# Kernel tuning notes

Hardware: AMD Instinct MI355X
Metric: run time of the kernel (lower is better)

## Reference

```python
import jax, jax.numpy as jnp
import numpy as np

N, TI, TO1 = 8, 200, 51
V, E, H, J, L = 1024, 512, 512, 512, 3
ENC_D = 512


def setup_inputs() -> dict:
    key = jax.random.key(0)
    ks = jax.random.split(key, 11)
    s = lambda k, shape, sc: jax.random.normal(k, shape, jnp.float32) * sc
    return {
        "enc_out": s(ks[0], (N, TI, ENC_D), 1.0),
        "tgt_pad": jax.random.randint(ks[1], (N, TO1), 0, V),
        "embed": s(ks[2], (V, E), 0.02),          # nn.Embedding weight
        "w_ih": s(ks[3], (L, 4 * H, E), 0.04),    # LSTM input-hidden (gate order i,f,g,o)
        "w_hh": s(ks[4], (L, 4 * H, H), 0.04),    # LSTM hidden-hidden
        "b_ih": s(ks[5], (L, 4 * H), 0.04),
        "b_hh": s(ks[6], (L, 4 * H), 0.04),
        "enc_w": s(ks[7], (J, ENC_D), 0.04),      # enc_proj (no bias)
        "dec_w": s(ks[8], (J, H), 0.04),          # dec_proj weight
        "dec_b": s(ks[9], (J,), 0.04),            # dec_proj bias
        "out_w": s(ks[10], (V, J), 0.04),         # output (no bias)
    }


def lstm_layer(x, wih, whh, bih, bhh):
    # x: [N, T, E] -> [N, T, H]; PyTorch LSTM gate order i, f, g, o
    n = x.shape[0]
    h0 = jnp.zeros((n, whh.shape[1]), x.dtype)
    c0 = jnp.zeros_like(h0)
    gin = jnp.einsum('nte,ge->ntg', x, wih) + bih + bhh  # precompute input contributions

    def step(carry, g_t):
        h, c = carry
        g = g_t + h @ whh.T
        i, f, gg, o = jnp.split(g, 4, axis=-1)
        c = jax.nn.sigmoid(f) * c + jax.nn.sigmoid(i) * jnp.tanh(gg)
        h = jax.nn.sigmoid(o) * jnp.tanh(c)
        return (h, c), h

    _, hs = jax.lax.scan(step, (h0, c0), jnp.swapaxes(gin, 0, 1))
    return jnp.swapaxes(hs, 0, 1)


def reference(enc_out, tgt_pad, embed, w_ih, w_hh, b_ih, b_hh, enc_w, dec_w, dec_b, out_w):
    # embedding lookup
    x = embed[tgt_pad]                                   # [N, To+1, E]
    # 3-layer unidirectional LSTM
    for l in range(w_ih.shape[0]):
        x = lstm_layer(x, w_ih[l], w_hh[l], b_ih[l], b_hh[l])
    # projections
    enc_p = jnp.einsum('ntd,jd->ntj', enc_out, enc_w)    # [N, Ti, J]
    dec_p = jnp.einsum('nud,jd->nuj', x, dec_w) + dec_b  # [N, To+1, J]
    # joint: broadcast add -> tanh -> output linear (no bias)
    add = enc_p[:, :, None, :] + dec_p[:, None, :, :]    # [N, Ti, To+1, J]
    return jnp.einsum('ntuj,vj->ntuv', jnp.tanh(add), out_w)  # [N, Ti, To+1, V]
```

## Files before the change

kernel.cpp:

```cpp
#include <hip/hip_runtime.h>
#include <cstdint>
#include <cstddef>

typedef __attribute__((ext_vector_type(4))) float f32x4;
typedef __attribute__((ext_vector_type(8))) short bf16x8;
typedef __attribute__((ext_vector_type(8))) unsigned short u16x8;
typedef __attribute__((ext_vector_type(4))) float float4v;
typedef __attribute__((ext_vector_type(2))) unsigned long long u64x2;
typedef unsigned long long ull;

#define NB   8
#define TIN  200
#define TO1  51
#define VSZ  1024
#define HSZ  512
static constexpr int MJOINT = NB * TIN * TO1;
static constexpr int MROWS  = TO1 * NB;

static constexpr size_t B_ENCBF = 0;
static constexpr size_t B_ENCW  = B_ENCBF + 1664ull*512*2;
static constexpr size_t B_DECW  = B_ENCW  + 512ull*512*2;
static constexpr size_t B_OUTW  = B_DECW  + 512ull*512*2;
static constexpr size_t B_WIH   = B_OUTW  + 1024ull*512*2;
static constexpr size_t B_WHH   = B_WIH   + 3ull*2048*512*2;
static constexpr size_t B_XTR   = B_WHH   + 3ull*2048*512*2;
static constexpr size_t B_BSUM  = B_XTR   + 4ull*408*512*2;
static constexpr size_t B_FLAGS = B_BSUM  + 3ull*2048*4;
static constexpr size_t B_ENCP  = B_FLAGS + 8192;
static constexpr size_t B_DECP  = B_ENCP  + 1664ull*512*4;
static constexpr size_t B_ABUF  = B_DECP  + 512ull*512*4;

__device__ __forceinline__ unsigned short f2bf(float f) {
  union { float f; unsigned u; } v; v.f = f;
  unsigned r = v.u + 0x7FFFu + ((v.u >> 16) & 1u);
  return (unsigned short)(r >> 16);
}
__device__ __forceinline__ float fast_tanh(float x) {
  float t = __expf(2.0f * x);
  return 1.0f - 2.0f / (t + 1.0f);
}
__device__ __forceinline__ float fast_sig(float x) {
  return 1.0f / (1.0f + __expf(-x));
}
__device__ __forceinline__ void gll16(const void* g, void* l) {
  __builtin_amdgcn_global_load_lds(
      (const __attribute__((address_space(1))) unsigned int*)g,
      (__attribute__((address_space(3))) unsigned int*)l, 16, 0, 0);
}
__device__ __forceinline__ void cvt8(const float* s, unsigned short* d) {
  const float4v* sp = (const float4v*)s;
  float4v x = sp[0], y = sp[1];
  u16x8 o;
  o[0]=f2bf(x[0]); o[1]=f2bf(x[1]); o[2]=f2bf(x[2]); o[3]=f2bf(x[3]);
  o[4]=f2bf(y[0]); o[5]=f2bf(y[1]); o[6]=f2bf(y[2]); o[7]=f2bf(y[3]);
  *(u16x8*)d = o;
}
#define ALOAD(P)     __hip_atomic_load((P), __ATOMIC_RELAXED, __HIP_MEMORY_SCOPE_AGENT)
#define ASTORE(P, V) __hip_atomic_store((P), (V), __ATOMIC_RELAXED, __HIP_MEMORY_SCOPE_AGENT)

static constexpr int N_ENC  = 102400;
static constexpr int N_ENCW = 32768;
static constexpr int N_DECW = 32768;
static constexpr int N_OUTW = 65536;
static constexpr int N_WIH  = 393216;
static constexpr int P0 = N_ENC, P1 = P0+N_ENCW, P2 = P1+N_DECW, P3 = P2+N_OUTW,
                     P4 = P3+N_WIH;

__global__ __launch_bounds__(256) void prep_all(const float* __restrict__ enc,
                                                const float* __restrict__ encw,
                                                const float* __restrict__ decw,
                                                const float* __restrict__ outw,
                                                const float* __restrict__ wih,
                                                const float* __restrict__ whh,
                                                const float* __restrict__ emb,
                                                const int* __restrict__ tgt,
                                                const float* __restrict__ bih,
                                                const float* __restrict__ bhh,
                                                unsigned short* __restrict__ d_enc,
                                                unsigned short* __restrict__ d_encw,
                                                unsigned short* __restrict__ d_decw,
                                                unsigned short* __restrict__ d_outw,
                                                unsigned short* __restrict__ d_wih,
                                                unsigned short* __restrict__ d_whh,
                                                unsigned short* __restrict__ x0,
                                                float* __restrict__ bsum,
                                                int* __restrict__ flags) {
  if (blockIdx.x == 0 && threadIdx.x < 97) flags[threadIdx.x * 16] = 0;
  if (blockIdx.x >= 4086) {
    int i = (blockIdx.x - 4086) * 2048 + threadIdx.x * 8;
#pragma unroll
    for (int k = 0; k < 8; ++k) bsum[i + k] = bih[i + k] + bhh[i + k];
    return;
  }
  if (blockIdx.x >= 3984) {
    int idx = (blockIdx.x - 3984) * 256 + threadIdx.x;
    if (idx >= MROWS * 64) return;
    int m = idx >> 6, kc = (idx & 63) * 8;
    int t = m >> 3, n = m & 7;
    int v = tgt[n * TO1 + t];
    cvt8(emb + (size_t)v * 512 + kc, x0 + (size_t)m * 512 + kc);
    return;
  }
  int i = blockIdx.x * 256 + threadIdx.x;
  const float* s; unsigned short* d; int rel;
  if      (i < P0) { s = enc;  d = d_enc;  rel = i; }
  else if (i < P1) { s = encw; d = d_encw; rel = i - P0; }
  else if (i < P2) { s = decw; d = d_decw; rel = i - P1; }
  else if (i < P3) { s = outw; d = d_outw; rel = i - P2; }
  else if (i < P4) { s = wih;  d = d_wih;  rel = i - P3; }
  else             { s = whh;  d = d_whh;  rel = i - P4; }
  cvt8(s + (size_t)rel * 8, d + (size_t)rel * 8);
}

__global__ __launch_bounds__(512) void gemm256(const unsigned short* __restrict__ A,
                                               const unsigned short* __restrict__ B,
                                               float* __restrict__ C,
                                               int M, int N, int K) {
  __shared__ __align__(16) unsigned short lds[2][2][16384];
  const int tid = threadIdx.x;
  const int wave = tid >> 6, lane = tid & 63;
  const int lr = lane & 15, lg = lane >> 4;
  const int wr = (wave >> 2) * 128;
  const int wc = (wave & 3) * 64;

  const int nwg = gridDim.x * gridDim.y;
  const int id = blockIdx.y * gridDim.x + blockIdx.x;
  const int q = nwg >> 3, r = nwg & 7, xcd = id & 7, rest = id >> 3;
  const int nid = (xcd < r ? xcd * (q + 1) : r * (q + 1) + (xcd - r) * q) + rest;
  const size_t n0 = (size_t)(nid % gridDim.x) * 256;
  const size_t m0 = (size_t)(nid / gridDim.x) * 256;

  f32x4 acc[8][4];
#pragma unroll
  for (int i = 0; i < 8; ++i)
#pragma unroll
    for (int j = 0; j < 4; ++j) acc[i][j] = (f32x4){0.f, 0.f, 0.f, 0.f};

#define STGH(bf, kt, h)                                                                 \
  do {                                                                                  \
    const unsigned short* SRC_ = ((h) < 2) ? A : B;                                     \
    const size_t base_ = ((h) < 2) ? m0 : n0;                                           \
    _Pragma("unroll") for (int u = 0; u < 2; ++u) {                                     \
      const int idx2 = u * 512 + tid;                                                   \
      const int rloc = (idx2 >> 3) + (((h) & 1) << 7);                                  \
      const int ch = (idx2 & 7) ^ (rloc & 7);                                           \
      gll16(SRC_ + (base_ + rloc) * (size_t)K + (kt) + ch * 8,                          \
            &lds[bf][(h) >> 1][((((h) & 1) << 10) + u * 512 + wave * 64) * 8]);         \
    }                                                                                   \
  } while (0)

  STGH(0, 0, 0); STGH(0, 0, 1); STGH(0, 0, 2); STGH(0, 0, 3);

  int cur = 0;
  for (int t = 0; t < 8; ++t) {
    const int nxt = cur ^ 1;
    const unsigned short* As_ = lds[cur][0];
    const unsigned short* Bs_ = lds[cur][1];
    bf16x8 b[4][2];
#pragma unroll
    for (int p = 0; p < 4; ++p) {
      if (t + 1 < 8) STGH(nxt, (t + 1) * 64, p);
      if (p == 0) {
        if (t + 1 < 8) asm volatile("s_waitcnt vmcnt(2)" ::: "memory");
        else           asm volatile("s_waitcnt vmcnt(0)" ::: "memory");
        __builtin_amdgcn_s_barrier();
#pragma unroll
        for (int j = 0; j < 4; ++j) {
          const int rb = wc + j * 16 + lr;
          const int sw = rb & 7;
          b[j][0] = *(const bf16x8*)&Bs_[rb * 64 + ((lg ^ sw) << 3)];
          b[j][1] = *(const bf16x8*)&Bs_[rb * 64 + (((4 + lg) ^ sw) << 3)];
        }
      }
      bf16x8 a[2][2];
#pragma unroll
      for (int i2 = 0; i2 < 2; ++i2) {
        const int ra = wr + (p * 2 + i2) * 16 + lr;
        const int swa = ra & 7;
        a[i2][0] = *(const bf16x8*)&As_[ra * 64 + ((lg ^ swa) << 3)];
        a[i2][1] = *(const bf16x8*)&As_[ra * 64 + (((4 + lg) ^ swa) << 3)];
      }
      __builtin_amdgcn_s_setprio(1);
#pragma unroll
      for (int i2 = 0; i2 < 2; ++i2) {
        const int i = p * 2 + i2;
#pragma unroll
        for (int j = 0; j < 4; ++j) {
          acc[i][j] = __builtin_amdgcn_mfma_f32_16x16x32_bf16(a[i2][0], b[j][0], acc[i][j], 0, 0, 0);
          acc[i][j] = __builtin_amdgcn_mfma_f32_16x16x32_bf16(a[i2][1], b[j][1], acc[i][j], 0, 0, 0);
        }
      }
      __builtin_amdgcn_s_setprio(0);
      __builtin_amdgcn_s_barrier();
    }
    cur = nxt;
  }
#undef STGH

#pragma unroll
  for (int i = 0; i < 8; ++i) {
#pragma unroll
    for (int q2 = 0; q2 < 4; ++q2) {
      const long m = (long)m0 + wr + i * 16 + lg * 4 + q2;
      if (m < M) {
        float* crow = C + (size_t)m * N + n0 + wc;
#pragma unroll
        for (int j = 0; j < 4; ++j) crow[j * 16 + lr] = acc[i][j][q2];
      }
    }
  }
}

__global__ __launch_bounds__(256) void mega_kernel(const unsigned short* __restrict__ wih,
                                                   const unsigned short* __restrict__ whh,
                                                   const float* __restrict__ bsum,
                                                   unsigned short* __restrict__ xtr,
                                                   int* __restrict__ flags,
                                                   const unsigned short* __restrict__ eA,
                                                   const unsigned short* __restrict__ eB,
                                                   float* __restrict__ eC,
                                                   const unsigned short* __restrict__ decw,
                                                   const float* __restrict__ dec_b,
                                                   const float* __restrict__ encp,
                                                   unsigned short* __restrict__ abuf) {
  __shared__ __align__(16) unsigned short w_s[64 * 1024];
  __shared__ __align__(16) unsigned short x_s[8 * 512];
  __shared__ __align__(16) unsigned short h_s[8 * 512];
  __shared__ float gates_s[4][8][16];

  const int tid = threadIdx.x;
  const int wave = tid >> 6, lane = tid & 63;
  const int lr = lane & 15, lg = lane >> 4;
  const int r7 = lr & 7;

  if (blockIdx.x >= 148) {
    const int wkr = blockIdx.x - 148;
    unsigned short* h3_s = x_s;
    float* decp_row = (float*)w_s;
    const unsigned short* xtr3 = xtr + 3ull * MROWS * 512;
#pragma unroll 1
    for (int k = 0; k < 4; ++k) {
      const int j = wkr + 102 * k;
      const int u = j >> 3;
      const int p = j & 7;
      if (wave == 0) {
        for (;;) {
          bool ok = true;
          if (lane < 32) ok = ALOAD(&flags[(64 + lane) * 16]) >= u + 1;
          else if (lane == 32) ok = ALOAD(&flags[96 * 16]) >= 52;
          if (__all(ok)) break;
          __builtin_amdgcn_s_sleep(1);
        }
      }
      __syncthreads();
      {
        const int sr2 = tid >> 5, sc2 = tid & 31;
        const ull* ph = (const ull*)(xtr3 + ((size_t)u * 8 + sr2) * 512);
#pragma unroll
        for (int k2 = 0; k2 < 2; ++k2) {
          const int c_ = sc2 + k2 * 32;
          ull v0 = ALOAD(ph + c_ * 2), v1 = ALOAD(ph + c_ * 2 + 1);
          *(u64x2*)&h3_s[sr2 * 512 + ((c_ ^ sr2) << 3)] = (u64x2){v0, v1};
        }
      }
      __syncthreads();
      {
        const int colbase = wave * 128;
#pragma unroll
        for (int ct = 0; ct < 8; ++ct) {
          f32x4 acc = (f32x4){0.f, 0.f, 0.f, 0.f};
          const int col = colbase + ct * 16 + lr;
#pragma unroll
          for (int c16 = 0; c16 < 16; ++c16) {
            const int cc = c16 * 4 + lg;
            bf16x8 av = *(const bf16x8*)&h3_s[r7 * 512 + ((cc ^ r7) << 3)];
            bf16x8 bv = *(const bf16x8*)&decw[(size_t)col * 512 + cc * 8];
            acc = __builtin_amdgcn_mfma_f32_16x16x32_bf16(av, bv, acc, 0, 0, 0);
          }
#pragma unroll
          for (int q2 = 0; q2 < 4; ++q2)
            if (lg * 4 + q2 == p) decp_row[col] = acc[q2] + dec_b[col];
        }
      }
      __syncthreads();
      {
        const int tr = tid >> 6;
        const int colc = (lane) * 8;
        for (int pass = 0; pass < 50; ++pass) {
          const int nt = p * 200 + pass * 4 + tr;
          const float4v* pe = (const float4v*)(encp + (size_t)nt * 512 + colc);
          float4v e0 = pe[0], e1 = pe[1];
          u16x8 o;
#pragma unroll
          for (int w2 = 0; w2 < 4; ++w2) {
            o[w2]     = f2bf(fast_tanh(e0[w2] + decp_row[colc + w2]));
            o[4 + w2] = f2bf(fast_tanh(e1[w2] + decp_row[colc + 4 + w2]));
          }
          *(u16x8*)&abuf[((size_t)nt * TO1 + u) * 512 + colc] = o;
        }
      }
      __syncthreads();
    }
    return;
  }

  if (blockIdx.x >= 96) {
    unsigned short* eld = w_s;
    const int g = blockIdx.x - 96;
    const int wm = (wave >> 1) * 64, wn = (wave & 1) * 64;
    const int xsl = (lg ^ (lr & 3)) << 3;
    const int nwg = 52;
    const int q = nwg >> 3, r = nwg & 7, xcd = g & 7, rest = g >> 3;
    const int nid = (xcd < r ? xcd * (q + 1) : r * (q + 1) + (xcd - r) * q) + rest;
    const size_t n0 = (size_t)(nid & 3) * 128;
    const size_t m0 = (size_t)(nid >> 2) * 128;

    f32x4 acc[4][4];
#pragma unroll
    for (int i = 0; i < 4; ++i)
#pragma unroll
      for (int j = 0; j < 4; ++j) acc[i][j] = (f32x4){0.f, 0.f, 0.f, 0.f};

#define ESTG(bf, kt)                                                                   \
    do {                                                                               \
      _Pragma("unroll") for (int u = 0; u < 2; ++u) {                                  \
        const int s = u * 256 + tid;                                                   \
        const int row_ = s >> 2;                                                       \
        const int ch = (s & 3) ^ (row_ & 3);                                           \
        gll16(eA + (m0 + row_) * 512 + (kt) + ch * 8,                                  \
              &eld[(bf) * 8192 + (u * 256 + wave * 64) * 8]);                          \
      }                                                                                \
      _Pragma("unroll") for (int u = 0; u < 2; ++u) {                                  \
        const int s = u * 256 + tid;                                                   \
        const int row_ = s >> 2;                                                       \
        const int ch = (s & 3) ^ (row_ & 3);                                           \
        gll16(eB + (n0 + row_) * 512 + (kt) + ch * 8,                                  \
              &eld[(bf) * 8192 + 4096 + (u * 256 + wave * 64) * 8]);                   \
      }                                                                                \
    } while (0)

    int cur = 0;
    ESTG(0, 0);
    for (int t = 0; t < 16; ++t) {
      if (t + 1 < 16) {
        ESTG(cur ^ 1, (t + 1) * 32);
        asm volatile("s_waitcnt vmcnt(4)" ::: "memory");
      } else {
        asm volatile("s_waitcnt vmcnt(0)" ::: "memory");
      }
      __builtin_amdgcn_s_barrier();
      const unsigned short* As_ = eld + cur * 8192;
      const unsigned short* Bs_ = As_ + 4096;
      bf16x8 a[4], b[4];
#pragma unroll
      for (int i = 0; i < 4; ++i) a[i] = *(const bf16x8*)&As_[(wm + i * 16 + lr) * 32 + xsl];
#pragma unroll
      for (int j = 0; j < 4; ++j) b[j] = *(const bf16x8*)&Bs_[(wn + j * 16 + lr) * 32 + xsl];
      __builtin_amdgcn_s_setprio(1);
#pragma unroll
      for (int i = 0; i < 4; ++i)
#pragma unroll
        for (int j = 0; j < 4; ++j)
          acc[i][j] = __builtin_amdgcn_mfma_f32_16x16x32_bf16(a[i], b[j], acc[i][j], 0, 0, 0);
      __builtin_amdgcn_s_setprio(0);
      __builtin_amdgcn_s_barrier();
      cur ^= 1;
    }
#undef ESTG

    const int rq = lg * 4;
#pragma unroll
    for (int j = 0; j < 4; ++j) {
      const int col = (int)n0 + wn + j * 16 + lr;
#pragma unroll
      for (int i = 0; i < 4; ++i) {
#pragma unroll
        for (int q2 = 0; q2 < 4; ++q2) {
          const long m = (long)m0 + wm + i * 16 + rq + q2;
          ASTORE(&eC[(size_t)m * 512 + col], acc[i][j][q2]);
        }
      }
    }
    asm volatile("s_waitcnt vmcnt(0)" ::: "memory");
    __syncthreads();
    if (tid == 0)
      __hip_atomic_fetch_add(&flags[96 * 16], 1, __ATOMIC_RELAXED, __HIP_MEMORY_SCOPE_AGENT);
    return;
  }

  const int l = blockIdx.x >> 5;
  const int b32 = blockIdx.x & 31;
  const int hid0 = b32 << 4;
  const int rw = wave * 16 + lr;

  {
    const int rl = tid >> 2;
    const int qt = tid & 3;
    const size_t R = (size_t)l * 2048 + (size_t)(rl >> 4) * 512 + hid0 + (rl & 15);
    const unsigned short* s0 = wih + R * 512;
    const unsigned short* s1 = whh + R * 512;
#pragma unroll
    for (int i = 0; i < 32; ++i) {
      int c = qt * 32 + i;
      bf16x8 wv = (c < 64) ? *(const bf16x8*)&s0[c * 8] : *(const bf16x8*)&s1[(c - 64) * 8];
      *(bf16x8*)&w_s[rl * 1024 + ((c ^ (rl & 7)) << 3)] = wv;
    }
  }
  const float bias = bsum[(size_t)l * 2048 + (size_t)wave * 512 + hid0 + lr];

  const unsigned short* xin = xtr + (size_t)l * MROWS * 512;
  unsigned short* xout = xtr + (size_t)(l + 1) * MROWS * 512;
  float c_reg = 0.f;
  const int srow = tid >> 5;
  const int sc = tid & 31;
  __syncthreads();

  f32x4 ax0, ax1;

  if (l > 0) {
    if (wave == 0) {
      for (;;) {
        bool ok_ = true;
        if (lane < 32)
          ok_ = ALOAD(&flags[((l - 1) * 32 + lane) * 16]) >= 1;
        if (__all(ok_)) break;
        __builtin_amdgcn_s_sleep(1);
      }
    }
  }
  __syncthreads();
  {
    const ull* px = (const ull*)(xin + (size_t)srow * 512);
#pragma unroll
    for (int k_ = 0; k_ < 2; ++k_) {
      const int c_ = sc + k_ * 32;
      ull v0 = ALOAD(px + c_ * 2), v1 = ALOAD(px + c_ * 2 + 1);
      *(u64x2*)&x_s[srow * 512 + ((c_ ^ srow) << 3)] = (u64x2){v0, v1};
    }
  }
  __syncthreads();
  ax0 = (f32x4){0.f, 0.f, 0.f, 0.f};
  ax1 = (f32x4){0.f, 0.f, 0.f, 0.f};
#pragma unroll
  for (int c16 = 0; c16 < 16; ++c16) {
    const int cc = c16 * 4 + lg;
    bf16x8 av = *(const bf16x8*)&x_s[r7 * 512 + ((cc ^ r7) << 3)];
    bf16x8 bv = *(const bf16x8*)&w_s[rw * 1024 + ((cc ^ r7) << 3)];
    if (c16 & 1) ax1 = __builtin_amdgcn_mfma_f32_16x16x32_bf16(av, bv, ax1, 0, 0, 0);
    else         ax0 = __builtin_amdgcn_mfma_f32_16x16x32_bf16(av, bv, ax0, 0, 0, 0);
  }

  for (int t = 0; t < TO1; ++t) {
    const bool doH = (t > 0);
    const bool doX = (t + 1 < TO1);
    if (doH || (doX && l > 0)) {
      if (wave == 0) {
        for (;;) {
          bool ok_ = true;
          if (lane < 32) {
            if (doH) ok_ = ALOAD(&flags[(l * 32 + lane) * 16]) >= t;
          } else {
            if (doX && l > 0)
              ok_ = ALOAD(&flags[((l - 1) * 32 + (lane - 32)) * 16]) >= t + 2;
          }
          if (__all(ok_)) break;
          __builtin_amdgcn_s_sleep(1);
        }
      }
    }
    __syncthreads();

    {
      ull vh[4], vx[4];
      const ull* ph = (const ull*)(xout + ((size_t)(t - 1) * 8 + srow) * 512);
      const ull* px = (const ull*)(xin + ((size_t)(t + 1) * 8 + srow) * 512);
#pragma unroll
      for (int k_ = 0; k_ < 2; ++k_) {
        const int c_ = sc + k_ * 32;
        if (doH) { vh[2 * k_] = ALOAD(ph + c_ * 2); vh[2 * k_ + 1] = ALOAD(ph + c_ * 2 + 1); }
        if (doX) { vx[2 * k_] = ALOAD(px + c_ * 2); vx[2 * k_ + 1] = ALOAD(px + c_ * 2 + 1); }
      }
#pragma unroll
      for (int k_ = 0; k_ < 2; ++k_) {
        const int c_ = sc + k_ * 32;
        if (doH) *(u64x2*)&h_s[srow * 512 + ((c_ ^ srow) << 3)] = (u64x2){vh[2 * k_], vh[2 * k_ + 1]};
        if (doX) *(u64x2*)&x_s[srow * 512 + ((c_ ^ srow) << 3)] = (u64x2){vx[2 * k_], vx[2 * k_ + 1]};
      }
    }
    __syncthreads();

    f32x4 acc0 = ax0, acc1 = ax1;
    if (doH) {
#pragma unroll
      for (int c16 = 0; c16 < 16; ++c16) {
        const int cc = c16 * 4 + lg;
        bf16x8 av = *(const bf16x8*)&h_s[r7 * 512 + ((cc ^ r7) << 3)];
        bf16x8 bv = *(const bf16x8*)&w_s[rw * 1024 + (((64 + cc) ^ r7) << 3)];
        if (c16 & 1) acc1 = __builtin_amdgcn_mfma_f32_16x16x32_bf16(av, bv, acc1, 0, 0, 0);
        else         acc0 = __builtin_amdgcn_mfma_f32_16x16x32_bf16(av, bv, acc0, 0, 0, 0);
      }
    }

    {
      f32x4 g = acc0 + acc1;
      const int nb4 = lg * 4;
#pragma unroll
      for (int q2 = 0; q2 < 4; ++q2) {
        int n = nb4 + q2;
        if (n < 8) gates_s[wave][n][lr] = g[q2] + bias;
      }
    }
    __syncthreads();
    if (tid < 128) {
      const int n = tid >> 4, j = tid & 15;
      float gi = gates_s[0][n][j], gf = gates_s[1][n][j];
      float gg = gates_s[2][n][j], go = gates_s[3][n][j];
      c_reg = fast_sig(gf) * c_reg + fast_sig(gi) * fast_tanh(gg);
      float ht = fast_sig(go) * fast_tanh(c_reg);
      float htn = __shfl_down(ht, 1);
      if (!(j & 1)) {
        unsigned pk = (unsigned)f2bf(ht) | ((unsigned)f2bf(htn) << 16);
        ASTORE((unsigned*)(xout + ((size_t)t * 8 + n) * 512 + hid0 + j), pk);
      }
    }
    asm volatile("s_waitcnt vmcnt(0)" ::: "memory");
    __syncthreads();
    if (tid == 0)
      ASTORE(&flags[(l * 32 + b32) * 16], t + 1);

    if (doX) {
      ax0 = (f32x4){0.f, 0.f, 0.f, 0.f};
      ax1 = (f32x4){0.f, 0.f, 0.f, 0.f};
#pragma unroll
      for (int c16 = 0; c16 < 16; ++c16) {
        const int cc = c16 * 4 + lg;
        bf16x8 av = *(const bf16x8*)&x_s[r7 * 512 + ((cc ^ r7) << 3)];
        bf16x8 bv = *(const bf16x8*)&w_s[rw * 1024 + ((cc ^ r7) << 3)];
        if (c16 & 1) ax1 = __builtin_amdgcn_mfma_f32_16x16x32_bf16(av, bv, ax1, 0, 0, 0);
        else         ax0 = __builtin_amdgcn_mfma_f32_16x16x32_bf16(av, bv, ax0, 0, 0, 0);
      }
    }
  }
}

extern "C" void kernel_launch(void* const* d_in, const int* in_sizes, int n_in,
                              void* d_out, int out_size, void* d_ws, size_t ws_size,
                              hipStream_t stream) {
  (void)in_sizes; (void)n_in; (void)out_size; (void)ws_size;
  const float* enc_out = (const float*)d_in[0];
  const int*   tgt     = (const int*)d_in[1];
  const float* embed   = (const float*)d_in[2];
  const float* w_ih    = (const float*)d_in[3];
  const float* w_hh    = (const float*)d_in[4];
  const float* b_ih    = (const float*)d_in[5];
  const float* b_hh    = (const float*)d_in[6];
  const float* enc_w   = (const float*)d_in[7];
  const float* dec_w   = (const float*)d_in[8];
  const float* dec_b   = (const float*)d_in[9];
  const float* out_w   = (const float*)d_in[10];

  char* ws = (char*)d_ws;
  unsigned short* enc_bf  = (unsigned short*)(ws + B_ENCBF);
  unsigned short* encw_bf = (unsigned short*)(ws + B_ENCW);
  unsigned short* decw_bf = (unsigned short*)(ws + B_DECW);
  unsigned short* outw_bf = (unsigned short*)(ws + B_OUTW);
  unsigned short* wih_bf  = (unsigned short*)(ws + B_WIH);
  unsigned short* whh_bf  = (unsigned short*)(ws + B_WHH);
  unsigned short* xtr     = (unsigned short*)(ws + B_XTR);
  float* bsum  = (float*)(ws + B_BSUM);
  int*   flags = (int*)(ws + B_FLAGS);
  float* encp  = (float*)(ws + B_ENCP);
  unsigned short* abuf = (unsigned short*)(ws + B_ABUF);
  float* Cout  = (float*)d_out;

  prep_all<<<4089, 256, 0, stream>>>(enc_out, enc_w, dec_w, out_w, w_ih, w_hh,
                                     embed, tgt, b_ih, b_hh,
                                     enc_bf, encw_bf, decw_bf, outw_bf, wih_bf, whh_bf,
                                     xtr, bsum, flags);

  mega_kernel<<<250, 256, 0, stream>>>(wih_bf, whh_bf, bsum, xtr, flags,
                                       enc_bf, encw_bf, encp,
                                       decw_bf, dec_b, encp, abuf);

  gemm256<<<dim3(4, 319), 512, 0, stream>>>(abuf, outw_bf, Cout, MJOINT, VSZ, 512);
}
```

Before: 325.7 us.

## Fuse output GEMM into persistent mega kernel with work-stealing tiles overlapping the LSTM

Removes the separate output GEMM launch and folds it into the persistent mega kernel. Blocks grab tiles through an atomic counter once they finish their LSTM, projection or joint roles. Each tile waits on per-timestep readiness flags, so the joint GEMM can start while later LSTM steps still run. The abuf layout becomes u-major so tiles map to contiguous timesteps, and blocks grow to 512 threads with only the first 256 doing the old work. This risks lower occupancy, spin-wait contention, and interference with the latency-critical recurrence.

```diff
diff --git a/kernel.cpp b/kernel.cpp
--- a/kernel.cpp
+++ b/kernel.cpp
@@ -16,6 +16,7 @@
 #define HSZ  512
 static constexpr int MJOINT = NB * TIN * TO1;
 static constexpr int MROWS  = TO1 * NB;
+static constexpr int NTK    = 319 * 4;
 
 static constexpr size_t B_ENCBF = 0;
 static constexpr size_t B_ENCW  = B_ENCBF + 1664ull*512*2;
@@ -57,6 +58,7 @@
 }
 #define ALOAD(P)     __hip_atomic_load((P), __ATOMIC_RELAXED, __HIP_MEMORY_SCOPE_AGENT)
 #define ASTORE(P, V) __hip_atomic_store((P), (V), __ATOMIC_RELAXED, __HIP_MEMORY_SCOPE_AGENT)
+#define AADD(P, V)   __hip_atomic_fetch_add((P), (V), __ATOMIC_RELAXED, __HIP_MEMORY_SCOPE_AGENT)
 
 static constexpr int N_ENC  = 102400;
 static constexpr int N_ENCW = 32768;
@@ -85,7 +87,10 @@
                                                 unsigned short* __restrict__ x0,
                                                 float* __restrict__ bsum,
                                                 int* __restrict__ flags) {
-  if (blockIdx.x == 0 && threadIdx.x < 97) flags[threadIdx.x * 16] = 0;
+  if (blockIdx.x == 0) {
+#pragma unroll
+    for (int k = 0; k < 8; ++k) flags[threadIdx.x * 8 + k] = 0;
+  }
   if (blockIdx.x >= 4086) {
     int i = (blockIdx.x - 4086) * 2048 + threadIdx.x * 8;
 #pragma unroll
@@ -112,106 +117,7 @@
   cvt8(s + (size_t)rel * 8, d + (size_t)rel * 8);
 }
 
-__global__ __launch_bounds__(512) void gemm256(const unsigned short* __restrict__ A,
-                                               const unsigned short* __restrict__ B,
-                                               float* __restrict__ C,
-                                               int M, int N, int K) {
-  __shared__ __align__(16) unsigned short lds[2][2][16384];
-  const int tid = threadIdx.x;
-  const int wave = tid >> 6, lane = tid & 63;
-  const int lr = lane & 15, lg = lane >> 4;
-  const int wr = (wave >> 2) * 128;
-  const int wc = (wave & 3) * 64;
-
-  const int nwg = gridDim.x * gridDim.y;
-  const int id = blockIdx.y * gridDim.x + blockIdx.x;
-  const int q = nwg >> 3, r = nwg & 7, xcd = id & 7, rest = id >> 3;
-  const int nid = (xcd < r ? xcd * (q + 1) : r * (q + 1) + (xcd - r) * q) + rest;
-  const size_t n0 = (size_t)(nid % gridDim.x) * 256;
-  const size_t m0 = (size_t)(nid / gridDim.x) * 256;
-
-  f32x4 acc[8][4];
-#pragma unroll
-  for (int i = 0; i < 8; ++i)
-#pragma unroll
-    for (int j = 0; j < 4; ++j) acc[i][j] = (f32x4){0.f, 0.f, 0.f, 0.f};
-
-#define STGH(bf, kt, h)                                                                 \
-  do {                                                                                  \
-    const unsigned short* SRC_ = ((h) < 2) ? A : B;                                     \
-    const size_t base_ = ((h) < 2) ? m0 : n0;                                           \
-    _Pragma("unroll") for (int u = 0; u < 2; ++u) {                                     \
-      const int idx2 = u * 512 + tid;                                                   \
-      const int rloc = (idx2 >> 3) + (((h) & 1) << 7);                                  \
-      const int ch = (idx2 & 7) ^ (rloc & 7);                                           \
-      gll16(SRC_ + (base_ + rloc) * (size_t)K + (kt) + ch * 8,                          \
-            &lds[bf][(h) >> 1][((((h) & 1) << 10) + u * 512 + wave * 64) * 8]);         \
-    }                                                                                   \
-  } while (0)
-
-  STGH(0, 0, 0); STGH(0, 0, 1); STGH(0, 0, 2); STGH(0, 0, 3);
-
-  int cur = 0;
-  for (int t = 0; t < 8; ++t) {
-    const int nxt = cur ^ 1;
-    const unsigned short* As_ = lds[cur][0];
-    const unsigned short* Bs_ = lds[cur][1];
-    bf16x8 b[4][2];
-#pragma unroll
-    for (int p = 0; p < 4; ++p) {
-      if (t + 1 < 8) STGH(nxt, (t + 1) * 64, p);
-      if (p == 0) {
-        if (t + 1 < 8) asm volatile("s_waitcnt vmcnt(2)" ::: "memory");
-        else           asm volatile("s_waitcnt vmcnt(0)" ::: "memory");
-        __builtin_amdgcn_s_barrier();
-#pragma unroll
-        for (int j = 0; j < 4; ++j) {
-          const int rb = wc + j * 16 + lr;
-          const int sw = rb & 7;
-          b[j][0] = *(const bf16x8*)&Bs_[rb * 64 + ((lg ^ sw) << 3)];
-          b[j][1] = *(const bf16x8*)&Bs_[rb * 64 + (((4 + lg) ^ sw) << 3)];
-        }
-      }
-      bf16x8 a[2][2];
-#pragma unroll
-      for (int i2 = 0; i2 < 2; ++i2) {
-        const int ra = wr + (p * 2 + i2) * 16 + lr;
-        const int swa = ra & 7;
-        a[i2][0] = *(const bf16x8*)&As_[ra * 64 + ((lg ^ swa) << 3)];
-        a[i2][1] = *(const bf16x8*)&As_[ra * 64 + (((4 + lg) ^ swa) << 3)];
-      }
-      __builtin_amdgcn_s_setprio(1);
-#pragma unroll
-      for (int i2 = 0; i2 < 2; ++i2) {
-        const int i = p * 2 + i2;
-#pragma unroll
-        for (int j = 0; j < 4; ++j) {
-          acc[i][j] = __builtin_amdgcn_mfma_f32_16x16x32_bf16(a[i2][0], b[j][0], acc[i][j], 0, 0, 0);
-          acc[i][j] = __builtin_amdgcn_mfma_f32_16x16x32_bf16(a[i2][1], b[j][1], acc[i][j], 0, 0, 0);
-        }
-      }
-      __builtin_amdgcn_s_setprio(0);
-      __builtin_amdgcn_s_barrier();
-    }
-    cur = nxt;
-  }
-#undef STGH
-
-#pragma unroll
-  for (int i = 0; i < 8; ++i) {
-#pragma unroll
-    for (int q2 = 0; q2 < 4; ++q2) {
-      const long m = (long)m0 + wr + i * 16 + lg * 4 + q2;
-      if (m < M) {
-        float* crow = C + (size_t)m * N + n0 + wc;
-#pragma unroll
-        for (int j = 0; j < 4; ++j) crow[j * 16 + lr] = acc[i][j][q2];
-      }
-    }
-  }
-}
-
-__global__ __launch_bounds__(256) void mega_kernel(const unsigned short* __restrict__ wih,
+__global__ __launch_bounds__(512) void mega_kernel(const unsigned short* __restrict__ wih,
                                                    const unsigned short* __restrict__ whh,
                                                    const float* __restrict__ bsum,
                                                    unsigned short* __restrict__ xtr,
@@ -222,11 +128,14 @@
                                                    const unsigned short* __restrict__ decw,
                                                    const float* __restrict__ dec_b,
                                                    const float* __restrict__ encp,
-                                                   unsigned short* __restrict__ abuf) {
+                                                   unsigned short* __restrict__ abuf,
+                                                   const unsigned short* __restrict__ outw,
+                                                   float* __restrict__ Cout) {
   __shared__ __align__(16) unsigned short w_s[64 * 1024];
   __shared__ __align__(16) unsigned short x_s[8 * 512];
   __shared__ __align__(16) unsigned short h_s[8 * 512];
   __shared__ float gates_s[4][8][16];
+  __shared__ int tk_s;
 
   const int tid = threadIdx.x;
   const int wave = tid >> 6, lane = tid & 63;
@@ -247,13 +156,13 @@
         for (;;) {
           bool ok = true;
           if (lane < 32) ok = ALOAD(&flags[(64 + lane) * 16]) >= u + 1;
-          else if (lane == 32) ok = ALOAD(&flags[96 * 16]) >= 52;
+          else if (lane == 32) ok = ALOAD(&flags[1536]) >= 52;
           if (__all(ok)) break;
           __builtin_amdgcn_s_sleep(1);
         }
       }
       __syncthreads();
-      {
+      if (tid < 256) {
         const int sr2 = tid >> 5, sc2 = tid & 31;
         const ull* ph = (const ull*)(xtr3 + ((size_t)u * 8 + sr2) * 512);
 #pragma unroll
@@ -264,7 +173,7 @@
         }
       }
       __syncthreads();
-      {
+      if (wave < 4) {
         const int colbase = wave * 128;
 #pragma unroll
         for (int ct = 0; ct < 8; ++ct) {
@@ -285,9 +194,9 @@
       __syncthreads();
       {
         const int tr = tid >> 6;
-        const int colc = (lane) * 8;
-        for (int pass = 0; pass < 50; ++pass) {
-          const int nt = p * 200 + pass * 4 + tr;
+        const int colc = lane * 8;
+        for (int pass = 0; pass < 25; ++pass) {
+          const int nt = p * 200 + pass * 8 + tr;
           const float4v* pe = (const float4v*)(encp + (size_t)nt * 512 + colc);
           float4v e0 = pe[0], e1 = pe[1];
           u16x8 o;
@@ -296,15 +205,17 @@
             o[w2]     = f2bf(fast_tanh(e0[w2] + decp_row[colc + w2]));
             o[4 + w2] = f2bf(fast_tanh(e1[w2] + decp_row[colc + 4 + w2]));
           }
-          *(u16x8*)&abuf[((size_t)nt * TO1 + u) * 512 + colc] = o;
-        }
-      }
-      __syncthreads();
-    }
-    return;
-  }
-
-  if (blockIdx.x >= 96) {
+          union { u16x8 v; ull d[2]; } cv; cv.v = o;
+          ull* pa = (ull*)&abuf[((size_t)u * 1600 + nt) * 512 + colc];
+          ASTORE(pa, cv.d[0]);
+          ASTORE(pa + 1, cv.d[1]);
+        }
+        asm volatile("s_waitcnt vmcnt(0)" ::: "memory");
+      }
+      __syncthreads();
+      if (tid == 0) AADD(&flags[1552 + u * 8], 1);
+    }
+  } else if (blockIdx.x >= 96) {
     unsigned short* eld = w_s;
     const int g = blockIdx.x - 96;
     const int wm = (wave >> 1) * 64, wn = (wave & 1) * 64;
@@ -340,197 +251,109 @@
     } while (0)
 
     int cur = 0;
-    ESTG(0, 0);
+    if (tid < 256) ESTG(0, 0);
     for (int t = 0; t < 16; ++t) {
       if (t + 1 < 16) {
-        ESTG(cur ^ 1, (t + 1) * 32);
+        if (tid < 256) ESTG(cur ^ 1, (t + 1) * 32);
         asm volatile("s_waitcnt vmcnt(4)" ::: "memory");
       } else {
         asm volatile("s_waitcnt vmcnt(0)" ::: "memory");
       }
       __builtin_amdgcn_s_barrier();
-      const unsigned short* As_ = eld + cur * 8192;
-      const unsigned short* Bs_ = As_ + 4096;
-      bf16x8 a[4], b[4];
-#pragma unroll
-      for (int i = 0; i < 4; ++i) a[i] = *(const bf16x8*)&As_[(wm + i * 16 + lr) * 32 + xsl];
-#pragma unroll
-      for (int j = 0; j < 4; ++j) b[j] = *(const bf16x8*)&Bs_[(wn + j * 16 + lr) * 32 + xsl];
-      __builtin_amdgcn_s_setprio(1);
-#pragma unroll
-      for (int i = 0; i < 4; ++i)
-#pragma unroll
-        for (int j = 0; j < 4; ++j)
-          acc[i][j] = __builtin_amdgcn_mfma_f32_16x16x32_bf16(a[i], b[j], acc[i][j], 0, 0, 0);
-      __builtin_amdgcn_s_setprio(0);
+      if (wave < 4) {
+        const unsigned short* As_ = eld + cur * 8192;
+        const unsigned short* Bs_ = As_ + 4096;
+        bf16x8 a[4], b[4];
+#pragma unroll
+        for (int i = 0; i < 4; ++i) a[i] = *(const bf16x8*)&As_[(wm + i * 16 + lr) * 32 + xsl];
+#pragma unroll
+        for (int j = 0; j < 4; ++j) b[j] = *(const bf16x8*)&Bs_[(wn + j * 16 + lr) * 32 + xsl];
+        __builtin_amdgcn_s_setprio(1);
+#pragma unroll
+        for (int i = 0; i < 4; ++i)
+#pragma unroll
+          for (int j = 0; j < 4; ++j)
+            acc[i][j] = __builtin_amdgcn_mfma_f32_16x16x32_bf16(a[i], b[j], acc[i][j], 0, 0, 0);
+        __builtin_amdgcn_s_setprio(0);
+      }
       __builtin_amdgcn_s_barrier();
       cur ^= 1;
     }
 #undef ESTG
 
-    const int rq = lg * 4;
-#pragma unroll
-    for (int j = 0; j < 4; ++j) {
-      const int col = (int)n0 + wn + j * 16 + lr;
-#pragma unroll
-      for (int i = 0; i < 4; ++i) {
-#pragma unroll
-        for (int q2 = 0; q2 < 4; ++q2) {
-          const long m = (long)m0 + wm + i * 16 + rq + q2;
-          ASTORE(&eC[(size_t)m * 512 + col], acc[i][j][q2]);
+    if (wave < 4) {
+      const int rq = lg * 4;
+#pragma unroll
+      for (int j = 0; j < 4; ++j) {
+        const int col = (int)n0 + wn + j * 16 + lr;
+#pragma unroll
+        for (int i = 0; i < 4; ++i) {
+#pragma unroll
+          for (int q2 = 0; q2 < 4; ++q2) {
+            const long m = (long)m0 + wm + i * 16 + rq + q2;
+            ASTORE(&eC[(size_t)m * 512 + col], acc[i][j][q2]);
+          }
         }
       }
     }
     asm volatile("s_waitcnt vmcnt(0)" ::: "memory");
     __syncthreads();
-    if (tid == 0)
-      __hip_atomic_fetch_add(&flags[96 * 16], 1, __ATOMIC_RELAXED, __HIP_MEMORY_SCOPE_AGENT);
-    return;
-  }
-
-  const int l = blockIdx.x >> 5;
-  const int b32 = blockIdx.x & 31;
-  const int hid0 = b32 << 4;
-  const int rw = wave * 16 + lr;
-
-  {
-    const int rl = tid >> 2;
-    const int qt = tid & 3;
-    const size_t R = (size_t)l * 2048 + (size_t)(rl >> 4) * 512 + hid0 + (rl & 15);
-    const unsigned short* s0 = wih + R * 512;
-    const unsigned short* s1 = whh + R * 512;
-#pragma unroll
-    for (int i = 0; i < 32; ++i) {
-      int c = qt * 32 + i;
-      bf16x8 wv = (c < 64) ? *(const bf16x8*)&s0[c * 8] : *(const bf16x8*)&s1[(c - 64) * 8];
-      *(bf16x8*)&w_s[rl * 1024 + ((c ^ (rl & 7)) << 3)] = wv;
-    }
-  }
-  const float bias = bsum[(size_t)l * 2048 + (size_t)wave * 512 + hid0 + lr];
-
-  const unsigned short* xin = xtr + (size_t)l * MROWS * 512;
-  unsigned short* xout = xtr + (size_t)(l + 1) * MROWS * 512;
-  float c_reg = 0.f;
-  const int srow = tid >> 5;
-  const int sc = tid & 31;
-  __syncthreads();
-
-  f32x4 ax0, ax1;
-
-  if (l > 0) {
-    if (wave == 0) {
-      for (;;) {
-        bool ok_ = true;
-        if (lane < 32)
-          ok_ = ALOAD(&flags[((l - 1) * 32 + lane) * 16]) >= 1;
-        if (__all(ok_)) break;
-        __builtin_amdgcn_s_sleep(1);
-      }
-    }
-  }
-  __syncthreads();
-  {
-    const ull* px = (const ull*)(xin + (size_t)srow * 512);
-#pragma unroll
-    for (int k_ = 0; k_ < 2; ++k_) {
-      const int c_ = sc + k_ * 32;
-      ull v0 = ALOAD(px + c_ * 2), v1 = ALOAD(px + c_ * 2 + 1);
-      *(u64x2*)&x_s[srow * 512 + ((c_ ^ srow) << 3)] = (u64x2){v0, v1};
-    }
-  }
-  __syncthreads();
-  ax0 = (f32x4){0.f, 0.f, 0.f, 0.f};
-  ax1 = (f32x4){0.f, 0.f, 0.f, 0.f};
-#pragma unroll
-  for (int c16 = 0; c16 < 16; ++c16) {
-    const int cc = c16 * 4 + lg;
-    bf16x8 av = *(const bf16x8*)&x_s[r7 * 512 + ((cc ^ r7) << 3)];
-    bf16x8 bv = *(const bf16x8*)&w_s[rw * 1024 + ((cc ^ r7) << 3)];
-    if (c16 & 1) ax1 = __builtin_amdgcn_mfma_f32_16x16x32_bf16(av, bv, ax1, 0, 0, 0);
-    else         ax0 = __builtin_amdgcn_mfma_f32_16x16x32_bf16(av, bv, ax0, 0, 0, 0);
-  }
-
-  for (int t = 0; t < TO1; ++t) {
-    const bool doH = (t > 0);
-    const bool doX = (t + 1 < TO1);
-    if (doH || (doX && l > 0)) {
+    if (tid == 0) AADD(&flags[1536], 1);
+  } else {
+    const int l = blockIdx.x >> 5;
+    const int b32 = blockIdx.x & 31;
+    const int hid0 = b32 << 4;
+    const int rw = wave * 16 + lr;
+
+    if (tid < 256) {
+      const int rl = tid >> 2;
+      const int qt = tid & 3;
+      const size_t R = (size_t)l * 2048 + (size_t)(rl >> 4) * 512 + hid0 + (rl & 15);
+      const unsigned short* s0 = wih + R * 512;
+      const unsigned short* s1 = whh + R * 512;
+#pragma unroll
+      for (int i = 0; i < 32; ++i) {
+        int c = qt * 32 + i;
+        bf16x8 wv = (c < 64) ? *(const bf16x8*)&s0[c * 8] : *(const bf16x8*)&s1[(c - 64) * 8];
+        *(bf16x8*)&w_s[rl * 1024 + ((c ^ (rl & 7)) << 3)] = wv;
+      }
+    }
+    float bias = 0.f;
+    if (wave < 4) bias = bsum[(size_t)l * 2048 + (size_t)wave * 512 + hid0 + lr];
+
+    const unsigned short* xin = xtr + (size_t)l * MROWS * 512;
+    unsigned short* xout = xtr + (size_t)(l + 1) * MROWS * 512;
+    float c_reg = 0.f;
+    const int srow = (tid >> 5) & 7;
+    const int sc = tid & 31;
+    __syncthreads();
+
+    f32x4 ax0 = (f32x4){0.f, 0.f, 0.f, 0.f};
+    f32x4 ax1 = (f32x4){0.f, 0.f, 0.f, 0.f};
+
+    if (l > 0) {
       if (wave == 0) {
         for (;;) {
           bool ok_ = true;
-          if (lane < 32) {
-            if (doH) ok_ = ALOAD(&flags[(l * 32 + lane) * 16]) >= t;
-          } else {
-            if (doX && l > 0)
-              ok_ = ALOAD(&flags[((l - 1) * 32 + (lane - 32)) * 16]) >= t + 2;
-          }
+          if (lane < 32)
+            ok_ = ALOAD(&flags[((l - 1) * 32 + lane) * 16]) >= 1;
           if (__all(ok_)) break;
           __builtin_amdgcn_s_sleep(1);
         }
       }
     }
     __syncthreads();
-
-    {
-      ull vh[4], vx[4];
-      const ull* ph = (const ull*)(xout + ((size_t)(t - 1) * 8 + srow) * 512);
-      const ull* px = (const ull*)(xin + ((size_t)(t + 1) * 8 + srow) * 512);
+    if (tid < 256) {
+      const ull* px = (const ull*)(xin + (size_t)srow * 512);
 #pragma unroll
       for (int k_ = 0; k_ < 2; ++k_) {
         const int c_ = sc + k_ * 32;
-        if (doH) { vh[2 * k_] = ALOAD(ph + c_ * 2); vh[2 * k_ + 1] = ALOAD(ph + c_ * 2 + 1); }
-        if (doX) { vx[2 * k_] = ALOAD(px + c_ * 2); vx[2 * k_ + 1] = ALOAD(px + c_ * 2 + 1); }
-      }
-#pragma unroll
-      for (int k_ = 0; k_ < 2; ++k_) {
-        const int c_ = sc + k_ * 32;
-        if (doH) *(u64x2*)&h_s[srow * 512 + ((c_ ^ srow) << 3)] = (u64x2){vh[2 * k_], vh[2 * k_ + 1]};
-        if (doX) *(u64x2*)&x_s[srow * 512 + ((c_ ^ srow) << 3)] = (u64x2){vx[2 * k_], vx[2 * k_ + 1]};
+        ull v0 = ALOAD(px + c_ * 2), v1 = ALOAD(px + c_ * 2 + 1);
+        *(u64x2*)&x_s[srow * 512 + ((c_ ^ srow) << 3)] = (u64x2){v0, v1};
       }
     }
     __syncthreads();
-
-    f32x4 acc0 = ax0, acc1 = ax1;
-    if (doH) {
-#pragma unroll
-      for (int c16 = 0; c16 < 16; ++c16) {
-        const int cc = c16 * 4 + lg;
-        bf16x8 av = *(const bf16x8*)&h_s[r7 * 512 + ((cc ^ r7) << 3)];
-        bf16x8 bv = *(const bf16x8*)&w_s[rw * 1024 + (((64 + cc) ^ r7) << 3)];
-        if (c16 & 1) acc1 = __builtin_amdgcn_mfma_f32_16x16x32_bf16(av, bv, acc1, 0, 0, 0);
-        else         acc0 = __builtin_amdgcn_mfma_f32_16x16x32_bf16(av, bv, acc0, 0, 0, 0);
-      }
-    }
-
-    {
-      f32x4 g = acc0 + acc1;
-      const int nb4 = lg * 4;
-#pragma unroll
-      for (int q2 = 0; q2 < 4; ++q2) {
-        int n = nb4 + q2;
-        if (n < 8) gates_s[wave][n][lr] = g[q2] + bias;
-      }
-    }
-    __syncthreads();
-    if (tid < 128) {
-      const int n = tid >> 4, j = tid & 15;
-      float gi = gates_s[0][n][j], gf = gates_s[1][n][j];
-      float gg = gates_s[2][n][j], go = gates_s[3][n][j];
-      c_reg = fast_sig(gf) * c_reg + fast_sig(gi) * fast_tanh(gg);
-      float ht = fast_sig(go) * fast_tanh(c_reg);
-      float htn = __shfl_down(ht, 1);
-      if (!(j & 1)) {
-        unsigned pk = (unsigned)f2bf(ht) | ((unsigned)f2bf(htn) << 16);
-        ASTORE((unsigned*)(xout + ((size_t)t * 8 + n) * 512 + hid0 + j), pk);
-      }
-    }
-    asm volatile("s_waitcnt vmcnt(0)" ::: "memory");
-    __syncthreads();
-    if (tid == 0)
-      ASTORE(&flags[(l * 32 + b32) * 16], t + 1);
-
-    if (doX) {
-      ax0 = (f32x4){0.f, 0.f, 0.f, 0.f};
-      ax1 = (f32x4){0.f, 0.f, 0.f, 0.f};
+    if (wave < 4) {
 #pragma unroll
       for (int c16 = 0; c16 < 16; ++c16) {
         const int cc = c16 * 4 + lg;
@@ -540,6 +363,209 @@
         else         ax0 = __builtin_amdgcn_mfma_f32_16x16x32_bf16(av, bv, ax0, 0, 0, 0);
       }
     }
+
+    for (int t = 0; t < TO1; ++t) {
+      const bool doH = (t > 0);
+      const bool doX = (t + 1 < TO1);
+      if (doH || (doX && l > 0)) {
+        if (wave == 0) {
+          for (;;) {
+            bool ok_ = true;
+            if (lane < 32) {
+              if (doH) ok_ = ALOAD(&flags[(l * 32 + lane) * 16]) >= t;
+            } else {
+              if (doX && l > 0)
+                ok_ = ALOAD(&flags[((l - 1) * 32 + (lane - 32)) * 16]) >= t + 2;
+            }
+            if (__all(ok_)) break;
+            __builtin_amdgcn_s_sleep(1);
+          }
+        }
+      }
+      __syncthreads();
+
+      if (tid < 256) {
+        ull vh[4], vx[4];
+        const ull* ph = (const ull*)(xout + ((size_t)(t - 1) * 8 + srow) * 512);
+        const ull* px = (const ull*)(xin + ((size_t)(t + 1) * 8 + srow) * 512);
+#pragma unroll
+        for (int k_ = 0; k_ < 2; ++k_) {
+          const int c_ = sc + k_ * 32;
+          if (doH) { vh[2 * k_] = ALOAD(ph + c_ * 2); vh[2 * k_ + 1] = ALOAD(ph + c_ * 2 + 1); }
+          if (doX) { vx[2 * k_] = ALOAD(px + c_ * 2); vx[2 * k_ + 1] = ALOAD(px + c_ * 2 + 1); }
+        }
+#pragma unroll
+        for (int k_ = 0; k_ < 2; ++k_) {
+          const int c_ = sc + k_ * 32;
+          if (doH) *(u64x2*)&h_s[srow * 512 + ((c_ ^ srow) << 3)] = (u64x2){vh[2 * k_], vh[2 * k_ + 1]};
+          if (doX) *(u64x2*)&x_s[srow * 512 + ((c_ ^ srow) << 3)] = (u64x2){vx[2 * k_], vx[2 * k_ + 1]};
+        }
+      }
+      __syncthreads();
+
+      f32x4 acc0 = ax0, acc1 = ax1;
+      if (doH && wave < 4) {
+#pragma unroll
+        for (int c16 = 0; c16 < 16; ++c16) {
+          const int cc = c16 * 4 + lg;
+          bf16x8 av = *(const bf16x8*)&h_s[r7 * 512 + ((cc ^ r7) << 3)];
+          bf16x8 bv = *(const bf16x8*)&w_s[rw * 1024 + (((64 + cc) ^ r7) << 3)];
+          if (c16 & 1) acc1 = __builtin_amdgcn_mfma_f32_16x16x32_bf16(av, bv, acc1, 0, 0, 0);
+          else         acc0 = __builtin_amdgcn_mfma_f32_16x16x32_bf16(av, bv, acc0, 0, 0, 0);
+        }
+      }
+
+      if (wave < 4) {
+        f32x4 g = acc0 + acc1;
+        const int nb4 = lg * 4;
+#pragma unroll
+        for (int q2 = 0; q2 < 4; ++q2) {
+          int n = nb4 + q2;
+          if (n < 8) gates_s[wave][n][lr] = g[q2] + bias;
+        }
+      }
+      __syncthreads();
+      if (tid < 128) {
+        const int n = tid >> 4, jj = tid & 15;
+        float gi = gates_s[0][n][jj], gf = gates_s[1][n][jj];
+        float gg = gates_s[2][n][jj], go = gates_s[3][n][jj];
+        c_reg = fast_sig(gf) * c_reg + fast_sig(gi) * fast_tanh(gg);
+        float ht = fast_sig(go) * fast_tanh(c_reg);
+        float htn = __shfl_down(ht, 1);
+        if (!(jj & 1)) {
+          unsigned pk = (unsigned)f2bf(ht) | ((unsigned)f2bf(htn) << 16);
+          ASTORE((unsigned*)(xout + ((size_t)t * 8 + n) * 512 + hid0 + jj), pk);
+        }
+      }
+      asm volatile("s_waitcnt vmcnt(0)" ::: "memory");
+      __syncthreads();
+      if (tid == 0)
+        ASTORE(&flags[(l * 32 + b32) * 16], t + 1);
+
+      if (doX && wave < 4) {
+        ax0 = (f32x4){0.f, 0.f, 0.f, 0.f};
+        ax1 = (f32x4){0.f, 0.f, 0.f, 0.f};
+#pragma unroll
+        for (int c16 = 0; c16 < 16; ++c16) {
+          const int cc = c16 * 4 + lg;
+          bf16x8 av = *(const bf16x8*)&x_s[r7 * 512 + ((cc ^ r7) << 3)];
+          bf16x8 bv = *(const bf16x8*)&w_s[rw * 1024 + ((cc ^ r7) << 3)];
+          if (c16 & 1) ax1 = __builtin_amdgcn_mfma_f32_16x16x32_bf16(av, bv, ax1, 0, 0, 0);
+          else         ax0 = __builtin_amdgcn_mfma_f32_16x16x32_bf16(av, bv, ax0, 0, 0, 0);
+        }
+      }
+    }
+  }
+
+  __syncthreads();
+  {
+    unsigned short* glds = w_s;
+    const int wr = (wave >> 2) * 128;
+    const int wc = (wave & 3) * 64;
+
+#define GOFF(bf, ab, idx) ((((bf) * 2 + (ab)) * 16384 + (idx)))
+#define GSTGH(bf, kt, h)                                                               \
+    do {                                                                               \
+      const unsigned short* SRC_ = ((h) < 2) ? abuf : outw;                            \
+      const size_t base_ = ((h) < 2) ? (size_t)mp0 : n0;                               \
+      _Pragma("unroll") for (int u2 = 0; u2 < 2; ++u2) {                               \
+        const int idx2 = u2 * 512 + tid;                                               \
+        const int rloc = (idx2 >> 3) + (((h) & 1) << 7);                               \
+        const int ch = (idx2 & 7) ^ (rloc & 7);                                        \
+        gll16(SRC_ + (base_ + rloc) * 512 + (kt) + ch * 8,                             \
+              &glds[GOFF(bf, (h) >> 1, ((((h) & 1) << 10) + u2 * 512 + wave * 64) * 8)]); \
+      }                                                                                \
+    } while (0)
+
+    for (;;) {
+      if (tid == 0) {
+        int tk = (int)AADD(&flags[1960], 1);
+        if (tk < NTK) {
+          const int m0_ = (tk >> 2) * 256;
+          const int ulo = m0_ / 1600;
+          int uhi = (m0_ + 255) / 1600; if (uhi > 50) uhi = 50;
+          while (ALOAD(&flags[1552 + ulo * 8]) < 8 || ALOAD(&flags[1552 + uhi * 8]) < 8)
+            __builtin_amdgcn_s_sleep(2);
+        }
+        tk_s = tk;
+      }
+      __syncthreads();
+      const int tk = tk_s;
+      if (tk >= NTK) break;
+      const int mp0 = (tk >> 2) * 256;
+      const size_t n0 = (size_t)(tk & 3) * 256;
+
+      f32x4 acc[8][4];
+#pragma unroll
+      for (int i = 0; i < 8; ++i)
+#pragma unroll
+        for (int j = 0; j < 4; ++j) acc[i][j] = (f32x4){0.f, 0.f, 0.f, 0.f};
+
+      GSTGH(0, 0, 0); GSTGH(0, 0, 1); GSTGH(0, 0, 2); GSTGH(0, 0, 3);
+
+      int cur = 0;
+      for (int t = 0; t < 8; ++t) {
+        const int nxt = cur ^ 1;
+        const unsigned short* As_ = &glds[GOFF(cur, 0, 0)];
+        const unsigned short* Bs_ = &glds[GOFF(cur, 1, 0)];
+        bf16x8 b[4][2];
+#pragma unroll
+        for (int p = 0; p < 4; ++p) {
+          if (t + 1 < 8) GSTGH(nxt, (t + 1) * 64, p);
+          if (p == 0) {
+            if (t + 1 < 8) asm volatile("s_waitcnt vmcnt(2)" ::: "memory");
+            else           asm volatile("s_waitcnt vmcnt(0)" ::: "memory");
+            __builtin_amdgcn_s_barrier();
+#pragma unroll
+            for (int j = 0; j < 4; ++j) {
+              const int rb = wc + j * 16 + lr;
+              const int sw = rb & 7;
+              b[j][0] = *(const bf16x8*)&Bs_[rb * 64 + ((lg ^ sw) << 3)];
+              b[j][1] = *(const bf16x8*)&Bs_[rb * 64 + (((4 + lg) ^ sw) << 3)];
+            }
+          }
+          bf16x8 a[2][2];
+#pragma unroll
+          for (int i2 = 0; i2 < 2; ++i2) {
+            const int ra = wr + (p * 2 + i2) * 16 + lr;
+            const int swa = ra & 7;
+            a[i2][0] = *(const bf16x8*)&As_[ra * 64 + ((lg ^ swa) << 3)];
+            a[i2][1] = *(const bf16x8*)&As_[ra * 64 + (((4 + lg) ^ swa) << 3)];
+          }
+          __builtin_amdgcn_s_setprio(1);
+#pragma unroll
+          for (int i2 = 0; i2 < 2; ++i2) {
+            const int i = p * 2 + i2;
+#pragma unroll
+            for (int j = 0; j < 4; ++j) {
+              acc[i][j] = __builtin_amdgcn_mfma_f32_16x16x32_bf16(a[i2][0], b[j][0], acc[i][j], 0, 0, 0);
+              acc[i][j] = __builtin_amdgcn_mfma_f32_16x16x32_bf16(a[i2][1], b[j][1], acc[i][j], 0, 0, 0);
+            }
+          }
+          __builtin_amdgcn_s_setprio(0);
+          __builtin_amdgcn_s_barrier();
+        }
+        cur = nxt;
+      }
+
+#pragma unroll
+      for (int i = 0; i < 8; ++i) {
+#pragma unroll
+        for (int q2 = 0; q2 < 4; ++q2) {
+          const long mp = (long)mp0 + wr + i * 16 + lg * 4 + q2;
+          if (mp < MJOINT) {
+            const int uu = (int)(mp / 1600);
+            const int nt = (int)(mp - (long)uu * 1600);
+            float* crow = Cout + ((size_t)nt * TO1 + uu) * VSZ + n0 + wc;
+#pragma unroll
+            for (int j = 0; j < 4; ++j) crow[j * 16 + lr] = acc[i][j][q2];
+          }
+        }
+      }
+      __syncthreads();
+    }
+#undef GSTGH
+#undef GOFF
   }
 }
 
@@ -578,9 +604,8 @@
                                      enc_bf, encw_bf, decw_bf, outw_bf, wih_bf, whh_bf,
                                      xtr, bsum, flags);
 
-  mega_kernel<<<250, 256, 0, stream>>>(wih_bf, whh_bf, bsum, xtr, flags,
+  mega_kernel<<<250, 512, 0, stream>>>(wih_bf, whh_bf, bsum, xtr, flags,
                                        enc_bf, encw_bf, encp,
-                                       decw_bf, dec_b, encp, abuf);
-
-  gemm256<<<dim3(4, 319), 512, 0, stream>>>(abuf, outw_bf, Cout, MJOINT, VSZ, 512);
-}
+                                       decw_bf, dec_b, encp, abuf,
+                                       outw_bf, Cout);
+}
```

Result: slower. 369.4 us (+13.4%).
